# Kernel tuning notes

Measured on AMD Instinct MI355X. Metric: run time of the kernel, lower is better.

The kernel has to match this reference:

```python
import jax, jax.numpy as jnp
import numpy as np

FILTERS = 256
B, H, W = 16, 64, 64
LN_EPS = 1e-5


def setup_inputs() -> dict:
    key = jax.random.key(0)
    ks = jax.random.split(key, 6)
    C = FILTERS
    scale = 1.0 / np.sqrt(C)  # kaiming-ish init for 1x1 convs
    return {
        "x": jax.random.normal(ks[0], (B, C, H, W), dtype=jnp.float32),
        "g": jax.random.normal(ks[1], (B, C, H, W), dtype=jnp.float32),
        "Wx": jax.random.normal(ks[2], (C, C), dtype=jnp.float32) * scale,
        "Wg": jax.random.normal(ks[3], (C, C), dtype=jnp.float32) * scale,
        "Wpsi": jax.random.normal(ks[4], (1, C), dtype=jnp.float32) * scale,
        "ln_gamma": jnp.ones((C,), dtype=jnp.float32),
        "ln_beta": jnp.zeros((C,), dtype=jnp.float32),
        "bxg": jnp.zeros((C,), dtype=jnp.float32),
        "bpsi": jnp.zeros((1,), dtype=jnp.float32),
    }


def reference(x, g, Wx, Wg, Wpsi, ln_gamma, ln_beta, bxg, bpsi):
    # 1x1 convs == per-pixel channel GEMMs: [B,C,H,W] x [O,C] -> [B,O,H,W]
    x_conv = jnp.einsum("bchw,oc->bohw", x, Wx)
    g_conv = jnp.einsum("bchw,oc->bohw", g, Wg)
    att = jax.nn.relu(x_conv + g_conv + bxg[None, :, None, None])
    # LayerNorm over channel dim (original permutes to NHWC, LN over last dim)
    mean = jnp.mean(att, axis=1, keepdims=True)
    var = jnp.mean(jnp.square(att - mean), axis=1, keepdims=True)
    att = (att - mean) * jax.lax.rsqrt(var + LN_EPS)
    att = att * ln_gamma[None, :, None, None] + ln_beta[None, :, None, None]
    # psi: 1x1 conv to single channel + bias, sigmoid gate
    att = jnp.einsum("bchw,oc->bohw", att, Wpsi) + bpsi[None, :, None, None]
    att = jax.nn.sigmoid(att)  # [B,1,H,W]
    return att * x
```

## Files before the change

kernel.cpp:

```cpp
#include <hip/hip_runtime.h>
#include <stdint.h>


typedef __bf16 bf16x8 __attribute__((ext_vector_type(8)));
typedef float f32x4 __attribute__((ext_vector_type(4)));

#define STR 40
#define LN_EPS 1e-5f

__device__ __forceinline__ uint16_t f2b(float f) {
    union { float f; uint32_t i; } v; v.f = f;
    uint32_t x = v.i;
    return (uint16_t)((x + 0x7FFFu + ((x >> 16) & 1u)) >> 16);
}

struct EpiShared {
    float red[3][4][64];
    float cpart[8];
};

union ALds {
    uint16_t a[2][2][64 * STR];
    EpiShared e;
};

__global__ void wconv_kernel(const float* __restrict__ Wx, const float* __restrict__ Wg,
                             uint16_t* __restrict__ ox, uint16_t* __restrict__ og) {
    const int i  = blockIdx.x * 256 + threadIdx.x;
    const int n  = i >> 6;
    const int k4 = (i & 63) * 4;
    const int it = k4 >> 5;
    const int kk = k4 & 31;
    const int dst = it * 8192 + n * 32 + kk;
    const float4 a = *(const float4*)&Wx[n * 256 + k4];
    const float4 b = *(const float4*)&Wg[n * 256 + k4];
    uint2 pa, pb;
    pa.x = (uint32_t)f2b(a.x) | ((uint32_t)f2b(a.y) << 16);
    pa.y = (uint32_t)f2b(a.z) | ((uint32_t)f2b(a.w) << 16);
    pb.x = (uint32_t)f2b(b.x) | ((uint32_t)f2b(b.y) << 16);
    pb.y = (uint32_t)f2b(b.z) | ((uint32_t)f2b(b.w) << 16);
    *(uint2*)&ox[dst] = pa;
    *(uint2*)&og[dst] = pb;
}

__device__ __forceinline__ void stage_load8(float av[8], const float* __restrict__ Asrc,
                                            size_t abase, int c0, int px) {
    #pragma unroll
    for (int c = 0; c < 8; ++c)
        av[c] = Asrc[abase + (size_t)(c0 + c) * 4096 + px];
}

__device__ __forceinline__ void stage_store8(const float av[8], uint16_t* dstrow, int c0) {
    uint4 w;
    w.x = (uint32_t)f2b(av[0]) | ((uint32_t)f2b(av[1]) << 16);
    w.y = (uint32_t)f2b(av[2]) | ((uint32_t)f2b(av[3]) << 16);
    w.z = (uint32_t)f2b(av[4]) | ((uint32_t)f2b(av[5]) << 16);
    w.w = (uint32_t)f2b(av[6]) | ((uint32_t)f2b(av[7]) << 16);
    *(uint4*)&dstrow[c0] = w;
}

__global__ __launch_bounds__(512, 6) void attgate_psi(
    const float* __restrict__ x,
    const float* __restrict__ g,
    const uint16_t* __restrict__ Wxb,
    const uint16_t* __restrict__ Wgb,
    const float* __restrict__ Wpsi,
    const float* __restrict__ gamma,
    const float* __restrict__ beta,
    const float* __restrict__ bxg,
    const float* __restrict__ bpsi,
    float* __restrict__ psi_g)
{
    __shared__ __align__(16) ALds u;

    const int t    = threadIdx.x;
    const int lane = t & 63;
    const int wv   = t >> 6;
    const int os   = wv & 3;
    const int ps   = wv >> 2;
    const int ln   = lane & 15;
    const int q    = lane >> 4;

    const int gp0  = blockIdx.x * 64;
    const int b    = gp0 >> 12;
    const int pix0 = gp0 & 4095;
    const size_t xbase = (size_t)b * (256 * 4096) + pix0;

    f32x4 acc[2][4];
    #pragma unroll
    for (int i = 0; i < 2; ++i)
        #pragma unroll
        for (int j = 0; j < 4; ++j)
            acc[i][j] = (f32x4){0.f, 0.f, 0.f, 0.f};

    const int at  = t & 255;
    const int px  = at & 63;
    const int cg  = at >> 6;
    const int c0  = cg * 8;
    const float* Asrc = (t < 256) ? x : g;
    const int tens    = (t < 256) ? 0 : 1;

    float av[8];
    stage_load8(av, Asrc, xbase, c0, px);
    stage_store8(av, &u.a[0][tens][px * STR], c0);

    const int fro = os * 64 + ln;

    for (int it = 0; it < 8; ++it) {
        __syncthreads();
        const int cur = it & 1;
        const uint16_t* Wxi = Wxb + it * 8192;
        const uint16_t* Wgi = Wgb + it * 8192;

        bf16x8 bx[4];
        #pragma unroll
        for (int nt = 0; nt < 4; ++nt)
            bx[nt] = *(const bf16x8*)&Wxi[(fro + nt * 16) * 32 + q * 8];

        if (it < 7)
            stage_load8(av, Asrc, xbase + (size_t)((it + 1) * 32) * 4096, c0, px);

        bf16x8 af[2];
        #pragma unroll
        for (int mt = 0; mt < 2; ++mt)
            af[mt] = *(const bf16x8*)&u.a[cur][0][(ps * 32 + mt * 16 + ln) * STR + q * 8];
        #pragma unroll
        for (int mt = 0; mt < 2; ++mt)
            #pragma unroll
            for (int nt = 0; nt < 4; ++nt)
                acc[mt][nt] = __builtin_amdgcn_mfma_f32_16x16x32_bf16(af[mt], bx[nt], acc[mt][nt], 0, 0, 0);

        bf16x8 bg[4];
        #pragma unroll
        for (int nt = 0; nt < 4; ++nt)
            bg[nt] = *(const bf16x8*)&Wgi[(fro + nt * 16) * 32 + q * 8];
        #pragma unroll
        for (int mt = 0; mt < 2; ++mt)
            af[mt] = *(const bf16x8*)&u.a[cur][1][(ps * 32 + mt * 16 + ln) * STR + q * 8];
        #pragma unroll
        for (int mt = 0; mt < 2; ++mt)
            #pragma unroll
            for (int nt = 0; nt < 4; ++nt)
                acc[mt][nt] = __builtin_amdgcn_mfma_f32_16x16x32_bf16(af[mt], bg[nt], acc[mt][nt], 0, 0, 0);

        if (it < 7)
            stage_store8(av, &u.a[cur ^ 1][tens][px * STR], c0);
    }

    __syncthreads();

    if (t < 256) {
        float a  = Wpsi[t] * gamma[t];
        float bb = Wpsi[t] * beta[t];
        #pragma unroll
        for (int off = 32; off; off >>= 1) {
            a  += __shfl_xor(a, off, 64);
            bb += __shfl_xor(bb, off, 64);
        }
        if (lane == 0) { u.e.cpart[wv] = a; u.e.cpart[4 + wv] = bb; }
    }

    float biasv[4], Ac[4];
    #pragma unroll
    for (int nt = 0; nt < 4; ++nt) {
        const int o = os * 64 + nt * 16 + ln;
        biasv[nt] = bxg[o];
        Ac[nt]    = Wpsi[o] * gamma[o];
    }
    __syncthreads();
    const float sumA = u.e.cpart[0] + u.e.cpart[1] + u.e.cpart[2] + u.e.cpart[3];
    const float sumB = u.e.cpart[4] + u.e.cpart[5] + u.e.cpart[6] + u.e.cpart[7];

    #pragma unroll
    for (int mt = 0; mt < 2; ++mt) {
        #pragma unroll
        for (int r = 0; r < 4; ++r) {
            float s = 0.f, ss = 0.f, tt = 0.f;
            #pragma unroll
            for (int nt = 0; nt < 4; ++nt) {
                float v = acc[mt][nt][r] + biasv[nt];
                v = fmaxf(v, 0.f);
                s += v; ss += v * v; tt += Ac[nt] * v;
            }
            #pragma unroll
            for (int off = 1; off < 16; off <<= 1) {
                s  += __shfl_xor(s,  off, 64);
                ss += __shfl_xor(ss, off, 64);
                tt += __shfl_xor(tt, off, 64);
            }
            if (ln == 0) {
                const int pix = ps * 32 + mt * 16 + q * 4 + r;
                u.e.red[0][os][pix] = s;
                u.e.red[1][os][pix] = ss;
                u.e.red[2][os][pix] = tt;
            }
        }
    }
    __syncthreads();

    if (t < 64) {
        const float s  = u.e.red[0][0][t] + u.e.red[0][1][t] + u.e.red[0][2][t] + u.e.red[0][3][t];
        const float ss = u.e.red[1][0][t] + u.e.red[1][1][t] + u.e.red[1][2][t] + u.e.red[1][3][t];
        const float tt = u.e.red[2][0][t] + u.e.red[2][1][t] + u.e.red[2][2][t] + u.e.red[2][3][t];
        const float mu   = s * (1.f / 256.f);
        const float var  = ss * (1.f / 256.f) - mu * mu;
        const float rstd = rsqrtf(var + LN_EPS);
        const float z    = rstd * (tt - mu * sumA) + sumB + bpsi[0];
        psi_g[gp0 + t] = 1.f / (1.f + __expf(-z));
    }
}

__global__ __launch_bounds__(256) void gate_mul(
    const float* __restrict__ x,
    const float* __restrict__ psi,
    float* __restrict__ out)
{
    const float4* __restrict__ x4  = (const float4*)x;
    float4* __restrict__ o4        = (float4*)out;
    int i = blockIdx.x * 256 + threadIdx.x;
    #pragma unroll 1
    for (; i < 4194304; i += 524288) {
        const int b   = i >> 18;
        const int rem = i & 262143;
        const int p4  = rem & 1023;
        const float4 pv = *(const float4*)&psi[(b << 12) + (p4 << 2)];
        const float4 xv = x4[i];
        float4 o;
        o.x = xv.x * pv.x; o.y = xv.y * pv.y; o.z = xv.z * pv.z; o.w = xv.w * pv.w;
        o4[i] = o;
    }
}

extern "C" void kernel_launch(void* const* d_in, const int* in_sizes, int n_in,
                              void* d_out, int out_size, void* d_ws, size_t ws_size,
                              hipStream_t stream) {
    const float* x    = (const float*)d_in[0];
    const float* g    = (const float*)d_in[1];
    const float* Wx   = (const float*)d_in[2];
    const float* Wg   = (const float*)d_in[3];
    const float* Wpsi = (const float*)d_in[4];
    const float* gam  = (const float*)d_in[5];
    const float* bet  = (const float*)d_in[6];
    const float* bxg  = (const float*)d_in[7];
    const float* bpsi = (const float*)d_in[8];
    float* out        = (float*)d_out;

    uint16_t* Wxb = (uint16_t*)d_ws;
    uint16_t* Wgb = (uint16_t*)((char*)d_ws + 131072);
    float*    psi = (float*)((char*)d_ws + 262144);

    wconv_kernel<<<dim3(64), dim3(256), 0, stream>>>(Wx, Wg, Wxb, Wgb);
    attgate_psi<<<dim3(1024), dim3(512), 0, stream>>>(
        x, g, Wxb, Wgb, Wpsi, gam, bet, bxg, bpsi, psi);
    gate_mul<<<dim3(2048), dim3(256), 0, stream>>>(x, psi, out);
}
```

Measured before the change: 218.0 us.

## Load full activation tile up front and drop per-iteration double-buffer syncs

Replaces the 8-stage double-buffered K loop with a single bulk load of all 64 channels per thread into registers, converts them to bf16 and stores the whole 64x256 tile to LDS, then runs the MFMA loop with only one barrier. This removes the seven per-iteration __syncthreads and exposes all global loads at once for memory-level parallelism. In exchange it needs 64 extra live registers and a larger LDS tile (about 67KB), so occupancy bound is lowered to 4 blocks and load/compute overlap across iterations is lost.

```diff
diff --git a/kernel.cpp b/kernel.cpp
--- a/kernel.cpp
+++ b/kernel.cpp
@@ -5,7 +5,7 @@
 typedef __bf16 bf16x8 __attribute__((ext_vector_type(8)));
 typedef float f32x4 __attribute__((ext_vector_type(4)));
 
-#define STR 40
+#define STR2 264
 #define LN_EPS 1e-5f
 
 __device__ __forceinline__ uint16_t f2b(float f) {
@@ -20,7 +20,7 @@
 };
 
 union ALds {
-    uint16_t a[2][2][64 * STR];
+    uint16_t a[2][64 * STR2];
     EpiShared e;
 };
 
@@ -43,23 +43,7 @@
     *(uint2*)&og[dst] = pb;
 }
 
-__device__ __forceinline__ void stage_load8(float av[8], const float* __restrict__ Asrc,
-                                            size_t abase, int c0, int px) {
-    #pragma unroll
-    for (int c = 0; c < 8; ++c)
-        av[c] = Asrc[abase + (size_t)(c0 + c) * 4096 + px];
-}
-
-__device__ __forceinline__ void stage_store8(const float av[8], uint16_t* dstrow, int c0) {
-    uint4 w;
-    w.x = (uint32_t)f2b(av[0]) | ((uint32_t)f2b(av[1]) << 16);
-    w.y = (uint32_t)f2b(av[2]) | ((uint32_t)f2b(av[3]) << 16);
-    w.z = (uint32_t)f2b(av[4]) | ((uint32_t)f2b(av[5]) << 16);
-    w.w = (uint32_t)f2b(av[6]) | ((uint32_t)f2b(av[7]) << 16);
-    *(uint4*)&dstrow[c0] = w;
-}
-
-__global__ __launch_bounds__(512, 6) void attgate_psi(
+__global__ __launch_bounds__(512, 4) void attgate_psi(
     const float* __restrict__ x,
     const float* __restrict__ g,
     const uint16_t* __restrict__ Wxb,
@@ -86,13 +70,6 @@
     const int pix0 = gp0 & 4095;
     const size_t xbase = (size_t)b * (256 * 4096) + pix0;
 
-    f32x4 acc[2][4];
-    #pragma unroll
-    for (int i = 0; i < 2; ++i)
-        #pragma unroll
-        for (int j = 0; j < 4; ++j)
-            acc[i][j] = (f32x4){0.f, 0.f, 0.f, 0.f};
-
     const int at  = t & 255;
     const int px  = at & 63;
     const int cg  = at >> 6;
@@ -100,15 +77,37 @@
     const float* Asrc = (t < 256) ? x : g;
     const int tens    = (t < 256) ? 0 : 1;
 
-    float av[8];
-    stage_load8(av, Asrc, xbase, c0, px);
-    stage_store8(av, &u.a[0][tens][px * STR], c0);
+    float av[64];
+    #pragma unroll
+    for (int it = 0; it < 8; ++it)
+        #pragma unroll
+        for (int c = 0; c < 8; ++c)
+            av[it * 8 + c] = Asrc[xbase + (size_t)(it * 32 + c0 + c) * 4096 + px];
+
+    uint16_t* dstrow = &u.a[tens][px * STR2];
+    #pragma unroll
+    for (int it = 0; it < 8; ++it) {
+        uint4 w;
+        w.x = (uint32_t)f2b(av[it*8+0]) | ((uint32_t)f2b(av[it*8+1]) << 16);
+        w.y = (uint32_t)f2b(av[it*8+2]) | ((uint32_t)f2b(av[it*8+3]) << 16);
+        w.z = (uint32_t)f2b(av[it*8+4]) | ((uint32_t)f2b(av[it*8+5]) << 16);
+        w.w = (uint32_t)f2b(av[it*8+6]) | ((uint32_t)f2b(av[it*8+7]) << 16);
+        *(uint4*)&dstrow[it * 32 + c0] = w;
+    }
+
+    f32x4 acc[2][4];
+    #pragma unroll
+    for (int i = 0; i < 2; ++i)
+        #pragma unroll
+        for (int j = 0; j < 4; ++j)
+            acc[i][j] = (f32x4){0.f, 0.f, 0.f, 0.f};
 
     const int fro = os * 64 + ln;
 
+    __syncthreads();
+
+    #pragma unroll
     for (int it = 0; it < 8; ++it) {
-        __syncthreads();
-        const int cur = it & 1;
         const uint16_t* Wxi = Wxb + it * 8192;
         const uint16_t* Wgi = Wgb + it * 8192;
 
@@ -117,13 +116,10 @@
         for (int nt = 0; nt < 4; ++nt)
             bx[nt] = *(const bf16x8*)&Wxi[(fro + nt * 16) * 32 + q * 8];
 
-        if (it < 7)
-            stage_load8(av, Asrc, xbase + (size_t)((it + 1) * 32) * 4096, c0, px);
-
         bf16x8 af[2];
         #pragma unroll
         for (int mt = 0; mt < 2; ++mt)
-            af[mt] = *(const bf16x8*)&u.a[cur][0][(ps * 32 + mt * 16 + ln) * STR + q * 8];
+            af[mt] = *(const bf16x8*)&u.a[0][(ps * 32 + mt * 16 + ln) * STR2 + it * 32 + q * 8];
         #pragma unroll
         for (int mt = 0; mt < 2; ++mt)
             #pragma unroll
@@ -136,15 +132,12 @@
             bg[nt] = *(const bf16x8*)&Wgi[(fro + nt * 16) * 32 + q * 8];
         #pragma unroll
         for (int mt = 0; mt < 2; ++mt)
-            af[mt] = *(const bf16x8*)&u.a[cur][1][(ps * 32 + mt * 16 + ln) * STR + q * 8];
+            af[mt] = *(const bf16x8*)&u.a[1][(ps * 32 + mt * 16 + ln) * STR2 + it * 32 + q * 8];
         #pragma unroll
         for (int mt = 0; mt < 2; ++mt)
             #pragma unroll
             for (int nt = 0; nt < 4; ++nt)
                 acc[mt][nt] = __builtin_amdgcn_mfma_f32_16x16x32_bf16(af[mt], bg[nt], acc[mt][nt], 0, 0, 0);
-
-        if (it < 7)
-            stage_store8(av, &u.a[cur ^ 1][tens][px * STR], c0);
     }
 
     __syncthreads();
```

Measured after the change: 222.9 us. 2.2% more time.

## Fuse gate multiply into attention kernel epilogue and raise occupancy hint

Applied to the files above, without the earlier changes.

The psi sigmoid is now kept in shared memory and each block multiplies its own 64-pixel slab of x across all 256 channels, then writes the output directly. This removes the separate gate_mul launch and the global psi round trip, and the x slab may still be in cache from the GEMM staging loads. The launch-bounds minimum waves per EU goes from 6 to 8, which can force register spilling. The epilogue writes use 64-byte contiguous rows per channel, a less coalesced pattern than the old flat streaming kernel.

```diff
diff --git a/kernel.cpp b/kernel.cpp
--- a/kernel.cpp
+++ b/kernel.cpp
@@ -16,6 +16,7 @@
 
 struct EpiShared {
     float red[3][4][64];
+    float psi[64];
     float cpart[8];
 };
 
@@ -59,7 +60,7 @@
     *(uint4*)&dstrow[c0] = w;
 }
 
-__global__ __launch_bounds__(512, 6) void attgate_psi(
+__global__ __launch_bounds__(512, 8) void attgate_kernel(
     const float* __restrict__ x,
     const float* __restrict__ g,
     const uint16_t* __restrict__ Wxb,
@@ -69,7 +70,7 @@
     const float* __restrict__ beta,
     const float* __restrict__ bxg,
     const float* __restrict__ bpsi,
-    float* __restrict__ psi_g)
+    float* __restrict__ out)
 {
     __shared__ __align__(16) ALds u;
 
@@ -206,28 +207,21 @@
         const float var  = ss * (1.f / 256.f) - mu * mu;
         const float rstd = rsqrtf(var + LN_EPS);
         const float z    = rstd * (tt - mu * sumA) + sumB + bpsi[0];
-        psi_g[gp0 + t] = 1.f / (1.f + __expf(-z));
-    }
-}
-
-__global__ __launch_bounds__(256) void gate_mul(
-    const float* __restrict__ x,
-    const float* __restrict__ psi,
-    float* __restrict__ out)
-{
-    const float4* __restrict__ x4  = (const float4*)x;
-    float4* __restrict__ o4        = (float4*)out;
-    int i = blockIdx.x * 256 + threadIdx.x;
-    #pragma unroll 1
-    for (; i < 4194304; i += 524288) {
-        const int b   = i >> 18;
-        const int rem = i & 262143;
-        const int p4  = rem & 1023;
-        const float4 pv = *(const float4*)&psi[(b << 12) + (p4 << 2)];
-        const float4 xv = x4[i];
+        u.e.psi[t] = 1.f / (1.f + __expf(-z));
+    }
+    __syncthreads();
+
+    const int pc = (t & 15) * 4;
+    const float4 pv = *(const float4*)&u.e.psi[pc];
+    const int crow = t >> 4;
+    #pragma unroll
+    for (int pass = 0; pass < 8; ++pass) {
+        const int c = pass * 32 + crow;
+        const size_t off = xbase + (size_t)c * 4096 + pc;
+        const float4 d = *(const float4*)&x[off];
         float4 o;
-        o.x = xv.x * pv.x; o.y = xv.y * pv.y; o.z = xv.z * pv.z; o.w = xv.w * pv.w;
-        o4[i] = o;
+        o.x = d.x * pv.x; o.y = d.y * pv.y; o.z = d.z * pv.z; o.w = d.w * pv.w;
+        *(float4*)&out[off] = o;
     }
 }
 
@@ -247,10 +241,8 @@
 
     uint16_t* Wxb = (uint16_t*)d_ws;
     uint16_t* Wgb = (uint16_t*)((char*)d_ws + 131072);
-    float*    psi = (float*)((char*)d_ws + 262144);
 
     wconv_kernel<<<dim3(64), dim3(256), 0, stream>>>(Wx, Wg, Wxb, Wgb);
-    attgate_psi<<<dim3(1024), dim3(512), 0, stream>>>(
-        x, g, Wxb, Wgb, Wpsi, gam, bet, bxg, bpsi, psi);
-    gate_mul<<<dim3(2048), dim3(256), 0, stream>>>(x, psi, out);
-}
+    attgate_kernel<<<dim3(1024), dim3(512), 0, stream>>>(
+        x, g, Wxb, Wgb, Wpsi, gam, bet, bxg, bpsi, out);
+}
```

After: 214.4 us. About the same (-1.7%).
